# Optimization experiments

Hardware: AMD Instinct MI355X
Metric: run time of the kernel (lower is better)

The kernel has to match this reference:

```python
import jax, jax.numpy as jnp
import numpy as np

# dims: batch, seq, latent dims, embed dims, hidden, num_flows, vocab
B, S, D, E, H, F, V = 64, 2048, 64, 64, 512, 4, 32000


def setup_inputs() -> dict:
    key = jax.random.key(0)
    ks = jax.random.split(key, 10)
    z = jax.random.normal(ks[0], (B, S, D), jnp.float32)
    categ = jax.random.randint(ks[1], (B, S), 0, V)
    embed = jax.random.normal(ks[2], (V, E), jnp.float32) * 0.1
    # ExtActNorm nets: SimpleLinearLayer(embed_dims -> 2*num_dims), one per flow
    actnorm_W = jax.random.normal(ks[3], (F, E, 2 * D), jnp.float32) * (1.0 / np.sqrt(E))
    actnorm_b = jnp.zeros((F, 2 * D), jnp.float32)
    # Invertible 1x1 convs: near-identity init keeps exp/logdet well conditioned
    conv_W = jnp.eye(D, dtype=jnp.float32)[None] + 0.05 * jax.random.normal(ks[4], (F, D, D), jnp.float32)
    # Coupling layers: scaling_factor (zeros, per torch init) + LinearNet MLP
    scaling_factor = jnp.zeros((F, D), jnp.float32)
    W0 = jax.random.normal(ks[5], (F, D + E, H), jnp.float32) * (1.0 / np.sqrt(D + E))
    b0 = jnp.zeros((F, H), jnp.float32)
    W1 = jax.random.normal(ks[6], (F, H, H), jnp.float32) * (1.0 / np.sqrt(H))
    b1 = jnp.zeros((F, H), jnp.float32)
    W2 = jax.random.normal(ks[7], (F, H, 2 * D), jnp.float32) * (0.05 / np.sqrt(H))
    b2 = jnp.zeros((F, 2 * D), jnp.float32)
    return dict(z=z, categ=categ, embed=embed, actnorm_W=actnorm_W, actnorm_b=actnorm_b,
                conv_W=conv_W, scaling_factor=scaling_factor,
                W0=W0, b0=b0, W1=W1, b1=b1, W2=W2, b2=b2)


def reference(z, categ, embed, actnorm_W, actnorm_b, conv_W, scaling_factor,
              W0, b0, W1, b1, W2, b2):
    # channel mask: first floor(D/2) channels are the conditioning half
    c_masked = D // 2
    mask = jnp.concatenate([jnp.ones((c_masked,), z.dtype), jnp.zeros((D - c_masked,), z.dtype)])
    mask = mask[None, None, :]                     # [1,1,D]
    ext = embed[categ]                             # [B,S,E] category embeddings (ext_input)
    ldj = jnp.zeros((z.shape[0],), z.dtype)
    for f in range(F):
        # --- ExtActNormFlow: params predicted from embedding ---
        nn_out = jnp.einsum('bse,eo->bso', ext, actnorm_W[f]) + actnorm_b[f]
        bias, scales = jnp.split(nn_out, 2, axis=2)
        scales = jnp.tanh(scales)
        z = (z + bias) * jnp.exp(scales)
        ldj = ldj + scales.sum(axis=(1, 2))
        # --- InvertibleConv (1x1 over channels) ---
        z = jnp.einsum('bsd,de->bse', z, conv_W[f])
        _, logabsdet = jnp.linalg.slogdet(conv_W[f])
        ldj = ldj + z.shape[1] * logabsdet
        # --- CouplingLayer with LinearNet(z*mask, ext) ---
        z_in = z * mask
        h = jnp.concatenate([z_in, ext], axis=-1)            # [B,S,D+E]
        h = jax.nn.gelu(h @ W0[f] + b0[f], approximate=False)
        h = jax.nn.gelu(h @ W1[f] + b1[f], approximate=False)
        nn_out = h @ W2[f] + b2[f]                           # [B,S,2D]
        nn_out = nn_out.reshape(nn_out.shape[:-1] + (D, 2))
        s, t = nn_out[..., 0], nn_out[..., 1]
        sf = jnp.exp(scaling_factor[f]).reshape(1, 1, D)
        s = jnp.tanh(s / jnp.maximum(sf, 1.0)) * sf          # soft-clamped scale
        s = s * (1.0 - mask)
        t = t * (1.0 - mask)
        z = (z + t) * jnp.exp(s)
        ldj = ldj + s.sum(axis=(1, 2))
    return z, ldj
```

## Files before the change

### kernel.cpp

```cpp
#include <hip/hip_runtime.h>
#include <math.h>

#define BB 64
#define SS 2048
#define DD 64
#define EE 64
#define HH 512
#define FF 4
#define NTOK (BB*SS)
#define ZELEMS (NTOK*DD)

#define PK2 1376256
#define AN_PER_FLOW 24576

typedef float f32x4 __attribute__((ext_vector_type(4)));
typedef float f32x2 __attribute__((ext_vector_type(2)));
typedef short s16x8 __attribute__((ext_vector_type(8)));
typedef unsigned int u32x2 __attribute__((ext_vector_type(2)));

__device__ __forceinline__ short f2b(float x) {
  unsigned u = __float_as_uint(x);
  u += 0x7fffu + ((u >> 16) & 1u);
  return (short)(u >> 16);
}
__device__ __forceinline__ float b2f(short h) {
  return __uint_as_float(((unsigned)(unsigned short)h) << 16);
}
__device__ __forceinline__ unsigned cvt_pk_bf16(float a, float b) {
  unsigned r;
  asm("v_cvt_pk_bf16_f32 %0, %1, %2" : "=v"(r) : "v"(a), "v"(b));
  return r;
}

__device__ __forceinline__ float tanh_fast(float x) {
  float e = __expf(2.0f * x);
  return 1.0f - 2.0f * __builtin_amdgcn_rcpf(e + 1.0f);
}
__device__ __forceinline__ float gelu_fast(float x) {
  float u = x * x;
  float p = x * fmaf(0.07135481283f, u, 1.5957691216f);
  float e = __expf(-p);
  return x * __builtin_amdgcn_rcpf(1.0f + e);
}

__global__ __launch_bounds__(256) void pack_kernel(
    const float* __restrict__ W0, const float* __restrict__ W1,
    const float* __restrict__ W2, short* __restrict__ wp,
    float* __restrict__ ldj)
{
  int gid = blockIdx.x * 256 + threadIdx.x;
  if (gid < BB) ldj[gid] = 0.f;
  int f = gid / 43008;
  if (f >= FF) return;
  int rem = gid - f * 43008;
  int tile = rem >> 6, lane = rem & 63;
  int q = lane >> 4, c = lane & 15;
  short out[8];
  short* dst;
  if (tile < 96) {
    int kt = tile >> 5, nt = tile & 31;
    #pragma unroll
    for (int j = 0; j < 8; j++) {
      int k = kt*32 + q*8 + j;
      int row = (k < 32) ? k : k + 32;
      out[j] = f2b(W0[f*65536 + row*512 + nt*16 + c]);
    }
    dst = wp + f*344064 + (tile*64 + lane)*8;
  } else if (tile < 608) {
    int tl = tile - 96;
    int kt = tl >> 5, nt = tl & 31;
    #pragma unroll
    for (int j = 0; j < 8; j++) {
      int k = kt*32 + q*8 + j;
      out[j] = f2b(W1[f*262144 + k*512 + nt*16 + c]);
    }
    dst = wp + f*344064 + 49152 + (tl*64 + lane)*8;
  } else {
    int tl = tile - 608;
    int kt = tl >> 2, nt = tl & 3;
    #pragma unroll
    for (int j = 0; j < 8; j++) {
      int k = kt*32 + q*8 + j;
      out[j] = f2b(W2[f*65536 + k*128 + 64 + nt*16 + c]);
    }
    dst = wp + f*344064 + 311296 + (tl*64 + lane)*8;
  }
  *(s16x8*)dst = *(s16x8*)out;
}

__global__ __launch_bounds__(256) void pack2_kernel(
    const float* __restrict__ Wa, const float* __restrict__ Wc,
    short* __restrict__ wp)
{
  int gid = blockIdx.x * 256 + threadIdx.x;
  int f = gid / 1536;
  if (f >= FF) return;
  int rem = gid - f * 1536;
  int u = rem >> 6, lane = rem & 63;
  int q = lane >> 4, c = lane & 15;
  short hi[8], lo[8];
  short* base = wp + PK2 + f*AN_PER_FLOW;
  short* dh; short* dl;
  if (u < 16) {
    int kt = u >> 3, nt = u & 7;
    #pragma unroll
    for (int j = 0; j < 8; j++) {
      float v = Wa[f*8192 + (kt*32 + q*8 + j)*128 + nt*16 + c];
      hi[j] = f2b(v);
      lo[j] = f2b(v - b2f(hi[j]));
    }
    dh = base + u*512 + lane*8;
    dl = base + 8192 + u*512 + lane*8;
  } else {
    int uc = u - 16;
    int kt = uc >> 2, nt = uc & 3;
    #pragma unroll
    for (int j = 0; j < 8; j++) {
      float v = Wc[f*4096 + (kt*32 + q*8 + j)*64 + nt*16 + c];
      hi[j] = f2b(v);
      lo[j] = f2b(v - b2f(hi[j]));
    }
    dh = base + 16384 + uc*512 + lane*8;
    dl = base + 16384 + 4096 + uc*512 + lane*8;
  }
  *(s16x8*)dh = *(s16x8*)hi;
  *(s16x8*)dl = *(s16x8*)lo;
}

__global__ __launch_bounds__(64) void slogdet_kernel(
    const float* __restrict__ convW, float* __restrict__ ldj)
{
  __shared__ float A[64*65];
  const int f = blockIdx.x;
  const int t = threadIdx.x;
  for (int i = 0; i < 64; i++) A[i*65 + t] = convW[f*4096 + i*64 + t];
  __syncthreads();
  float lad = 0.f;
  for (int k = 0; k < 64; k++) {
    float v = (t >= k) ? fabsf(A[t*65 + k]) : -1.f;
    int p = t;
    #pragma unroll
    for (int off = 32; off; off >>= 1) {
      float ov = __shfl_down(v, off);
      int  op = __shfl_down(p, off);
      if (ov > v) { v = ov; p = op; }
    }
    p = __shfl(p, 0);
    __syncthreads();
    if (p != k) {
      float tmp = A[k*65 + t];
      A[k*65 + t] = A[p*65 + t];
      A[p*65 + t] = tmp;
    }
    __syncthreads();
    float piv = A[k*65 + k];
    lad += logf(fabsf(piv));
    float m = (t > k) ? A[t*65 + k] / piv : 0.f;
    __syncthreads();
    if (t > k) {
      for (int c = k+1; c < 64; c++)
        A[t*65 + c] = fmaf(-m, A[k*65 + c], A[t*65 + c]);
    }
    __syncthreads();
  }
  atomicAdd(&ldj[t], (float)SS * lad);
}

__global__ __launch_bounds__(512, 4) void flow_kernel(
    const float* __restrict__ z_in, float* __restrict__ zout,
    const int* __restrict__ categ, const float* __restrict__ embed,
    const float* __restrict__ ba, const short* __restrict__ wp,
    const float* __restrict__ b0, const float* __restrict__ b1,
    const float* __restrict__ b2, const float* __restrict__ scal,
    float* __restrict__ ldj)
{
  extern __shared__ char smem[];
  float* zf = (float*)smem;
  short* hs = (short*)(smem + 16384);
  short* ExtH = hs;
  short* ExtL = hs + 4096;
  short* ehp  = hs + 8192;
  short* elp  = hs + 12288;
  short* zb   = hs + 16384;

  const int t    = threadIdx.x;
  const int tok0 = blockIdx.x * 64;
  const int lane = t & 63;
  const int w    = __builtin_amdgcn_readfirstlane(t >> 6);
  const int q    = lane >> 4, c16 = lane & 15;
  const int swz  = (c16 & 7) << 3;
  const int zswz = (c16 & 7) << 2;
  const f32x4 vzero = {0.f, 0.f, 0.f, 0.f};

  #pragma unroll
  for (int it = 0; it < 2; it++) {
    int idx = t + it*512;
    int r = idx >> 4, c4 = (idx & 15) * 4;
    f32x4 v = *(const f32x4*)&z_in[(tok0 + r)*64 + c4];
    *(f32x4*)&zf[r*64 + (c4 ^ ((r & 7) << 2))] = v;
  }

  float lsum = 0.f;

  for (int f = 0; f < FF; f++) {
    const short* base = wp + PK2 + f*AN_PER_FLOW;
    const short* w0p  = wp + f*344064;
    const short* w1p  = w0p + 49152;
    const short* w2p  = w0p + 311296;

    __syncthreads();

    #pragma unroll
    for (int it = 0; it < 2; it++) {
      int idx = t + it*512;
      int r = idx >> 4, c4 = (idx & 15) * 4;
      int sw = (r & 7) << 3;
      f32x4 v = *(const f32x4*)&embed[categ[tok0 + r]*64 + c4];
      unsigned h01 = cvt_pk_bf16(v[0], v[1]);
      unsigned h23 = cvt_pk_bf16(v[2], v[3]);
      float r0 = v[0] - __uint_as_float(h01 << 16);
      float r1 = v[1] - __uint_as_float(h01 & 0xffff0000u);
      float r2 = v[2] - __uint_as_float(h23 << 16);
      float r3 = v[3] - __uint_as_float(h23 & 0xffff0000u);
      u32x2 hv = {h01, h23};
      u32x2 lv = {cvt_pk_bf16(r0, r1), cvt_pk_bf16(r2, r3)};
      *(u32x2*)&ExtH[r*64 + (c4 ^ sw)] = hv;
      *(u32x2*)&ExtL[r*64 + (c4 ^ sw)] = lv;
    }
    __syncthreads();

    const int ntb  = w & 3;
    const int rowg = w >> 2;
    const int db   = ntb*16 + q*4;

    f32x4 aB[2], aS[2];
    aB[0] = vzero; aB[1] = vzero; aS[0] = vzero; aS[1] = vzero;
    #pragma unroll
    for (int kt = 0; kt < 2; kt++) {
      s16x8 bhB = *(const s16x8*)&base[(kt*8 + ntb)*512 + lane*8];
      s16x8 blB = *(const s16x8*)&base[8192 + (kt*8 + ntb)*512 + lane*8];
      s16x8 bhS = *(const s16x8*)&base[(kt*8 + ntb + 4)*512 + lane*8];
      s16x8 blS = *(const s16x8*)&base[8192 + (kt*8 + ntb + 4)*512 + lane*8];
      #pragma unroll
      for (int r = 0; r < 2; r++) {
        int row = (rowg*2 + r)*16 + c16;
        s16x8 ah = *(const s16x8*)&ExtH[row*64 + ((kt*32 + q*8) ^ swz)];
        s16x8 al = *(const s16x8*)&ExtL[row*64 + ((kt*32 + q*8) ^ swz)];
        aB[r] = __builtin_amdgcn_mfma_f32_16x16x32_bf16(bhB, ah, aB[r], 0,0,0);
        aB[r] = __builtin_amdgcn_mfma_f32_16x16x32_bf16(blB, ah, aB[r], 0,0,0);
        aB[r] = __builtin_amdgcn_mfma_f32_16x16x32_bf16(bhB, al, aB[r], 0,0,0);
        aS[r] = __builtin_amdgcn_mfma_f32_16x16x32_bf16(bhS, ah, aS[r], 0,0,0);
        aS[r] = __builtin_amdgcn_mfma_f32_16x16x32_bf16(blS, ah, aS[r], 0,0,0);
        aS[r] = __builtin_amdgcn_mfma_f32_16x16x32_bf16(bhS, al, aS[r], 0,0,0);
      }
    }

    {
      f32x4 bB4 = *(const f32x4*)&ba[f*128 + db];
      f32x4 bS4 = *(const f32x4*)&ba[f*128 + 64 + db];
      #pragma unroll
      for (int r = 0; r < 2; r++) {
        int row = (rowg*2 + r)*16 + c16;
        f32x4 zv = *(const f32x4*)&zf[row*64 + (db ^ zswz)];
        float zp[4];
        #pragma unroll
        for (int i = 0; i < 4; i++) {
          float s = tanh_fast(aS[r][i] + bS4[i]);
          lsum += s;
          zp[i] = (zv[i] + aB[r][i] + bB4[i]) * __expf(s);
        }
        unsigned h01 = cvt_pk_bf16(zp[0], zp[1]);
        unsigned h23 = cvt_pk_bf16(zp[2], zp[3]);
        float r0 = zp[0] - __uint_as_float(h01 << 16);
        float r1 = zp[1] - __uint_as_float(h01 & 0xffff0000u);
        float r2 = zp[2] - __uint_as_float(h23 << 16);
        float r3 = zp[3] - __uint_as_float(h23 & 0xffff0000u);
        u32x2 hv = {h01, h23};
        u32x2 lv = {cvt_pk_bf16(r0, r1), cvt_pk_bf16(r2, r3)};
        *(u32x2*)&ehp[row*64 + (db ^ swz)] = hv;
        *(u32x2*)&elp[row*64 + (db ^ swz)] = lv;
      }
    }
    __syncthreads();

    {
      f32x4 ac[2];
      ac[0] = vzero; ac[1] = vzero;
      #pragma unroll
      for (int kt = 0; kt < 2; kt++) {
        s16x8 bh = *(const s16x8*)&base[16384 + (kt*4 + ntb)*512 + lane*8];
        s16x8 bl = *(const s16x8*)&base[16384 + 4096 + (kt*4 + ntb)*512 + lane*8];
        #pragma unroll
        for (int r = 0; r < 2; r++) {
          int row = (rowg*2 + r)*16 + c16;
          s16x8 ah = *(const s16x8*)&ehp[row*64 + ((kt*32 + q*8) ^ swz)];
          s16x8 al = *(const s16x8*)&elp[row*64 + ((kt*32 + q*8) ^ swz)];
          ac[r] = __builtin_amdgcn_mfma_f32_16x16x32_bf16(bh, ah, ac[r], 0,0,0);
          ac[r] = __builtin_amdgcn_mfma_f32_16x16x32_bf16(bl, ah, ac[r], 0,0,0);
          ac[r] = __builtin_amdgcn_mfma_f32_16x16x32_bf16(bh, al, ac[r], 0,0,0);
        }
      }
      #pragma unroll
      for (int r = 0; r < 2; r++) {
        int row = (rowg*2 + r)*16 + c16;
        *(f32x4*)&zf[row*64 + (db ^ zswz)] = ac[r];
        u32x2 pv = {cvt_pk_bf16(ac[r][0], ac[r][1]),
                    cvt_pk_bf16(ac[r][2], ac[r][3])};
        *(u32x2*)&zb[row*64 + (db ^ swz)] = pv;
      }
    }
    __syncthreads();

    f32x4 acc[4][4];

    #pragma unroll
    for (int rt = 0; rt < 4; rt++)
      #pragma unroll
      for (int nl = 0; nl < 4; nl++) acc[rt][nl] = vzero;
    #pragma unroll
    for (int kt = 0; kt < 3; kt++) {
      s16x8 a[4];
      #pragma unroll
      for (int rt = 0; rt < 4; rt++) {
        int row = rt*16 + c16;
        a[rt] = (kt == 0)
          ? *(const s16x8*)&zb[row*64 + ((q*8) ^ swz)]
          : *(const s16x8*)&ExtH[row*64 + (((kt-1)*32 + q*8) ^ swz)];
      }
      #pragma unroll
      for (int nl = 0; nl < 4; nl++) {
        s16x8 b = *(const s16x8*)&w0p[((kt*32 + w*4 + nl)*64 + lane)*8];
        #pragma unroll
        for (int rt = 0; rt < 4; rt++)
          acc[rt][nl] = __builtin_amdgcn_mfma_f32_16x16x32_bf16(b, a[rt], acc[rt][nl], 0,0,0);
      }
    }
    __syncthreads();
    #pragma unroll
    for (int nl = 0; nl < 4; nl++) {
      int nt = w*4 + nl;
      f32x4 bias = *(const f32x4*)&b0[f*512 + nt*16 + q*4];
      #pragma unroll
      for (int rt = 0; rt < 4; rt++) {
        float g0 = gelu_fast(acc[rt][nl][0] + bias[0]);
        float g1 = gelu_fast(acc[rt][nl][1] + bias[1]);
        float g2 = gelu_fast(acc[rt][nl][2] + bias[2]);
        float g3 = gelu_fast(acc[rt][nl][3] + bias[3]);
        u32x2 pv = {cvt_pk_bf16(g0, g1), cvt_pk_bf16(g2, g3)};
        *(u32x2*)&hs[(rt*16 + c16)*512 + ((nt*16 + q*4) ^ swz)] = pv;
      }
    }
    __syncthreads();

    #pragma unroll
    for (int rt = 0; rt < 4; rt++)
      #pragma unroll
      for (int nl = 0; nl < 4; nl++) acc[rt][nl] = vzero;
    {
      s16x8 bcur[4];
      #pragma unroll
      for (int nl = 0; nl < 4; nl++)
        bcur[nl] = *(const s16x8*)&w1p[((w*4 + nl)*64 + lane)*8];
      #pragma unroll 2
      for (int kt = 0; kt < 16; kt++) {
        const int ktn = (kt + 1) & 15;
        s16x8 a[4];
        #pragma unroll
        for (int rt = 0; rt < 4; rt++)
          a[rt] = *(const s16x8*)&hs[(rt*16 + c16)*512 + ((kt*32 + q*8) ^ swz)];
        #pragma unroll
        for (int nl = 0; nl < 4; nl++) {
          s16x8 bn = *(const s16x8*)&w1p[((ktn*32 + w*4 + nl)*64 + lane)*8];
          #pragma unroll
          for (int rt = 0; rt < 4; rt++)
            acc[rt][nl] = __builtin_amdgcn_mfma_f32_16x16x32_bf16(bcur[nl], a[rt], acc[rt][nl], 0,0,0);
          bcur[nl] = bn;
        }
      }
    }
    __syncthreads();
    #pragma unroll
    for (int nl = 0; nl < 4; nl++) {
      int nt = w*4 + nl;
      f32x4 bias = *(const f32x4*)&b1[f*512 + nt*16 + q*4];
      #pragma unroll
      for (int rt = 0; rt < 4; rt++) {
        float g0 = gelu_fast(acc[rt][nl][0] + bias[0]);
        float g1 = gelu_fast(acc[rt][nl][1] + bias[1]);
        float g2 = gelu_fast(acc[rt][nl][2] + bias[2]);
        float g3 = gelu_fast(acc[rt][nl][3] + bias[3]);
        u32x2 pv = {cvt_pk_bf16(g0, g1), cvt_pk_bf16(g2, g3)};
        *(u32x2*)&hs[(rt*16 + c16)*512 + ((nt*16 + q*4) ^ swz)] = pv;
      }
    }
    __syncthreads();

    {
      const int ntc = w & 3;
      const int rtb = w >> 2;
      f32x4 a2[2];
      a2[0] = vzero; a2[1] = vzero;
      s16x8 b2cur = *(const s16x8*)&w2p[(ntc*64 + lane)*8];
      #pragma unroll 2
      for (int kt = 0; kt < 16; kt++) {
        const int ktn = (kt + 1) & 15;
        s16x8 b2nxt = *(const s16x8*)&w2p[((ktn*4 + ntc)*64 + lane)*8];
        s16x8 x0 = *(const s16x8*)&hs[(rtb*16 + c16)*512 + ((kt*32 + q*8) ^ swz)];
        s16x8 x1 = *(const s16x8*)&hs[((rtb + 2)*16 + c16)*512 + ((kt*32 + q*8) ^ swz)];
        a2[0] = __builtin_amdgcn_mfma_f32_16x16x32_bf16(b2cur, x0, a2[0], 0,0,0);
        a2[1] = __builtin_amdgcn_mfma_f32_16x16x32_bf16(b2cur, x1, a2[1], 0,0,0);
        b2cur = b2nxt;
      }
      const int ccb = 64 + ntc*16 + q*4;
      f32x4 b2v = *(const f32x4*)&b2[f*128 + ccb];
      const int d0 = ccb >> 1;
      f32x2 sc = *(const f32x2*)&scal[f*64 + d0];
      float sf0 = __expf(sc[0]); float mr0 = __builtin_amdgcn_rcpf(fmaxf(sf0, 1.0f));
      float sf1 = __expf(sc[1]); float mr1 = __builtin_amdgcn_rcpf(fmaxf(sf1, 1.0f));
      #pragma unroll
      for (int u = 0; u < 2; u++) {
        int row = (rtb + u*2)*16 + c16;
        int zi = row*64 + (d0 ^ zswz);
        f32x2 zv = *(f32x2*)&zf[zi];
        float s0 = tanh_fast((a2[u][0] + b2v[0]) * mr0) * sf0;
        float s1 = tanh_fast((a2[u][2] + b2v[2]) * mr1) * sf1;
        zv[0] = (zv[0] + (a2[u][1] + b2v[1])) * __expf(s0);
        zv[1] = (zv[1] + (a2[u][3] + b2v[3])) * __expf(s1);
        *(f32x2*)&zf[zi] = zv;
        lsum += s0 + s1;
      }
    }
  }

  __syncthreads();

  #pragma unroll
  for (int it = 0; it < 2; it++) {
    int idx = t + it*512;
    int r = idx >> 4, c4 = (idx & 15) * 4;
    f32x4 v = *(const f32x4*)&zf[r*64 + (c4 ^ ((r & 7) << 2))];
    *(f32x4*)&zout[(tok0 + r)*64 + c4] = v;
  }

  #pragma unroll
  for (int off = 32; off; off >>= 1) lsum += __shfl_xor(lsum, off);
  if (lane == 0) atomicAdd(&ldj[tok0 >> 11], lsum);
}

extern "C" void kernel_launch(void* const* d_in, const int* in_sizes, int n_in,
                              void* d_out, int out_size, void* d_ws, size_t ws_size,
                              hipStream_t stream) {
  (void)in_sizes; (void)n_in; (void)out_size; (void)ws_size;
  const float* z_in  = (const float*)d_in[0];
  const int*   categ = (const int*)  d_in[1];
  const float* embed = (const float*)d_in[2];
  const float* Wa    = (const float*)d_in[3];
  const float* ba    = (const float*)d_in[4];
  const float* Wc    = (const float*)d_in[5];
  const float* scal  = (const float*)d_in[6];
  const float* W0    = (const float*)d_in[7];
  const float* b0    = (const float*)d_in[8];
  const float* W1    = (const float*)d_in[9];
  const float* b1    = (const float*)d_in[10];
  const float* W2    = (const float*)d_in[11];
  const float* b2    = (const float*)d_in[12];

  float* zbuf = (float*)d_out;
  float* ldj  = zbuf + ZELEMS;
  short* wp   = (short*)d_ws;

  hipFuncSetAttribute(reinterpret_cast<const void*>(flow_kernel),
                      hipFuncAttributeMaxDynamicSharedMemorySize, 81920);

  pack_kernel<<<672, 256, 0, stream>>>(W0, W1, W2, wp, ldj);
  pack2_kernel<<<24, 256, 0, stream>>>(Wa, Wc, wp);
  slogdet_kernel<<<4, 64, 0, stream>>>(Wc, ldj);
  flow_kernel<<<NTOK/64, 512, 81920, stream>>>(
      z_in, zbuf, categ, embed, ba, wp, b0, b1, b2, scal, ldj);
}
```

Baseline: 1.029 ms.

## Split MLP row tiles into two passes to halve accumulator registers

The layer-0 and layer-1 GEMMs now run in two passes of 32 rows each with 2x4 accumulators instead of one pass over 64 rows with 4x4, which cuts live accumulator registers to help the occupancy target of the launch bounds. The bf16 copy of z is dropped and converted on the fly from the fp32 z buffer, and the shared-memory regions for ext and z are moved. In exchange, weight fragments for layers 0 and 1 are loaded twice per flow, and the layer-1 pass must sync before writing into the shared hidden buffer that the other pass still reads.

```diff
diff --git a/kernel.cpp b/kernel.cpp
--- a/kernel.cpp
+++ b/kernel.cpp
@@ -177,11 +177,10 @@
   extern __shared__ char smem[];
   float* zf = (float*)smem;
   short* hs = (short*)(smem + 16384);
-  short* ExtH = hs;
-  short* ExtL = hs + 4096;
-  short* ehp  = hs + 8192;
-  short* elp  = hs + 12288;
-  short* zb   = hs + 16384;
+  short* ehp  = hs + 16384;
+  short* ExtH = hs + 20480;
+  short* ExtL = hs + 24576;
+  short* elp  = hs + 28672;
 
   const int t    = threadIdx.x;
   const int tok0 = blockIdx.x * 64;
@@ -304,59 +303,69 @@
       for (int r = 0; r < 2; r++) {
         int row = (rowg*2 + r)*16 + c16;
         *(f32x4*)&zf[row*64 + (db ^ zswz)] = ac[r];
-        u32x2 pv = {cvt_pk_bf16(ac[r][0], ac[r][1]),
-                    cvt_pk_bf16(ac[r][2], ac[r][3])};
-        *(u32x2*)&zb[row*64 + (db ^ swz)] = pv;
-      }
-    }
-    __syncthreads();
-
-    f32x4 acc[4][4];
-
-    #pragma unroll
-    for (int rt = 0; rt < 4; rt++)
-      #pragma unroll
-      for (int nl = 0; nl < 4; nl++) acc[rt][nl] = vzero;
-    #pragma unroll
-    for (int kt = 0; kt < 3; kt++) {
-      s16x8 a[4];
-      #pragma unroll
-      for (int rt = 0; rt < 4; rt++) {
-        int row = rt*16 + c16;
-        a[rt] = (kt == 0)
-          ? *(const s16x8*)&zb[row*64 + ((q*8) ^ swz)]
-          : *(const s16x8*)&ExtH[row*64 + (((kt-1)*32 + q*8) ^ swz)];
-      }
+      }
+    }
+    __syncthreads();
+
+    #pragma unroll 1
+    for (int pass = 0; pass < 2; pass++) {
+      f32x4 acc[2][4];
+      #pragma unroll
+      for (int rt = 0; rt < 2; rt++)
+        #pragma unroll
+        for (int nl = 0; nl < 4; nl++) acc[rt][nl] = vzero;
+      #pragma unroll
+      for (int kt = 0; kt < 3; kt++) {
+        s16x8 a[2];
+        #pragma unroll
+        for (int rt = 0; rt < 2; rt++) {
+          int row = (pass*2 + rt)*16 + c16;
+          if (kt == 0) {
+            f32x4 v0 = *(const f32x4*)&zf[row*64 + ((q*8) ^ zswz)];
+            f32x4 v1 = *(const f32x4*)&zf[row*64 + ((q*8 + 4) ^ zswz)];
+            union { unsigned u[4]; s16x8 v; } cv;
+            cv.u[0] = cvt_pk_bf16(v0[0], v0[1]);
+            cv.u[1] = cvt_pk_bf16(v0[2], v0[3]);
+            cv.u[2] = cvt_pk_bf16(v1[0], v1[1]);
+            cv.u[3] = cvt_pk_bf16(v1[2], v1[3]);
+            a[rt] = cv.v;
+          } else {
+            a[rt] = *(const s16x8*)&ExtH[row*64 + (((kt-1)*32 + q*8) ^ swz)];
+          }
+        }
+        #pragma unroll
+        for (int nl = 0; nl < 4; nl++) {
+          s16x8 b = *(const s16x8*)&w0p[((kt*32 + w*4 + nl)*64 + lane)*8];
+          acc[0][nl] = __builtin_amdgcn_mfma_f32_16x16x32_bf16(b, a[0], acc[0][nl], 0,0,0);
+          acc[1][nl] = __builtin_amdgcn_mfma_f32_16x16x32_bf16(b, a[1], acc[1][nl], 0,0,0);
+        }
+      }
+      if (pass == 1) __syncthreads();
       #pragma unroll
       for (int nl = 0; nl < 4; nl++) {
-        s16x8 b = *(const s16x8*)&w0p[((kt*32 + w*4 + nl)*64 + lane)*8];
-        #pragma unroll
-        for (int rt = 0; rt < 4; rt++)
-          acc[rt][nl] = __builtin_amdgcn_mfma_f32_16x16x32_bf16(b, a[rt], acc[rt][nl], 0,0,0);
-      }
-    }
-    __syncthreads();
-    #pragma unroll
-    for (int nl = 0; nl < 4; nl++) {
-      int nt = w*4 + nl;
-      f32x4 bias = *(const f32x4*)&b0[f*512 + nt*16 + q*4];
-      #pragma unroll
-      for (int rt = 0; rt < 4; rt++) {
-        float g0 = gelu_fast(acc[rt][nl][0] + bias[0]);
-        float g1 = gelu_fast(acc[rt][nl][1] + bias[1]);
-        float g2 = gelu_fast(acc[rt][nl][2] + bias[2]);
-        float g3 = gelu_fast(acc[rt][nl][3] + bias[3]);
-        u32x2 pv = {cvt_pk_bf16(g0, g1), cvt_pk_bf16(g2, g3)};
-        *(u32x2*)&hs[(rt*16 + c16)*512 + ((nt*16 + q*4) ^ swz)] = pv;
-      }
-    }
-    __syncthreads();
-
-    #pragma unroll
-    for (int rt = 0; rt < 4; rt++)
-      #pragma unroll
-      for (int nl = 0; nl < 4; nl++) acc[rt][nl] = vzero;
-    {
+        int nt = w*4 + nl;
+        f32x4 bias = *(const f32x4*)&b0[f*512 + nt*16 + q*4];
+        #pragma unroll
+        for (int rt = 0; rt < 2; rt++) {
+          int row = (pass*2 + rt)*16 + c16;
+          float g0 = gelu_fast(acc[rt][nl][0] + bias[0]);
+          float g1 = gelu_fast(acc[rt][nl][1] + bias[1]);
+          float g2 = gelu_fast(acc[rt][nl][2] + bias[2]);
+          float g3 = gelu_fast(acc[rt][nl][3] + bias[3]);
+          u32x2 pv = {cvt_pk_bf16(g0, g1), cvt_pk_bf16(g2, g3)};
+          *(u32x2*)&hs[row*512 + ((nt*16 + q*4) ^ swz)] = pv;
+        }
+      }
+    }
+    __syncthreads();
+
+    #pragma unroll 1
+    for (int pass = 0; pass < 2; pass++) {
+      f32x4 acc[2][4];
+      #pragma unroll
+      for (int rt = 0; rt < 2; rt++)
+        #pragma unroll
+        for (int nl = 0; nl < 4; nl++) acc[rt][nl] = vzero;
       s16x8 bcur[4];
       #pragma unroll
       for (int nl = 0; nl < 4; nl++)
@@ -364,33 +373,33 @@
       #pragma unroll 2
       for (int kt = 0; kt < 16; kt++) {
         const int ktn = (kt + 1) & 15;
-        s16x8 a[4];
-        #pragma unroll
-        for (int rt = 0; rt < 4; rt++)
-          a[rt] = *(const s16x8*)&hs[(rt*16 + c16)*512 + ((kt*32 + q*8) ^ swz)];
+        s16x8 a[2];
+        #pragma unroll
+        for (int rt = 0; rt < 2; rt++)
+          a[rt] = *(const s16x8*)&hs[((pass*2 + rt)*16 + c16)*512 + ((kt*32 + q*8) ^ swz)];
         #pragma unroll
         for (int nl = 0; nl < 4; nl++) {
           s16x8 bn = *(const s16x8*)&w1p[((ktn*32 + w*4 + nl)*64 + lane)*8];
-          #pragma unroll
-          for (int rt = 0; rt < 4; rt++)
-            acc[rt][nl] = __builtin_amdgcn_mfma_f32_16x16x32_bf16(bcur[nl], a[rt], acc[rt][nl], 0,0,0);
+          acc[0][nl] = __builtin_amdgcn_mfma_f32_16x16x32_bf16(bcur[nl], a[0], acc[0][nl], 0,0,0);
+          acc[1][nl] = __builtin_amdgcn_mfma_f32_16x16x32_bf16(bcur[nl], a[1], acc[1][nl], 0,0,0);
           bcur[nl] = bn;
         }
       }
-    }
-    __syncthreads();
-    #pragma unroll
-    for (int nl = 0; nl < 4; nl++) {
-      int nt = w*4 + nl;
-      f32x4 bias = *(const f32x4*)&b1[f*512 + nt*16 + q*4];
-      #pragma unroll
-      for (int rt = 0; rt < 4; rt++) {
-        float g0 = gelu_fast(acc[rt][nl][0] + bias[0]);
-        float g1 = gelu_fast(acc[rt][nl][1] + bias[1]);
-        float g2 = gelu_fast(acc[rt][nl][2] + bias[2]);
-        float g3 = gelu_fast(acc[rt][nl][3] + bias[3]);
-        u32x2 pv = {cvt_pk_bf16(g0, g1), cvt_pk_bf16(g2, g3)};
-        *(u32x2*)&hs[(rt*16 + c16)*512 + ((nt*16 + q*4) ^ swz)] = pv;
+      __syncthreads();
+      #pragma unroll
+      for (int nl = 0; nl < 4; nl++) {
+        int nt = w*4 + nl;
+        f32x4 bias = *(const f32x4*)&b1[f*512 + nt*16 + q*4];
+        #pragma unroll
+        for (int rt = 0; rt < 2; rt++) {
+          int row = (pass*2 + rt)*16 + c16;
+          float g0 = gelu_fast(acc[rt][nl][0] + bias[0]);
+          float g1 = gelu_fast(acc[rt][nl][1] + bias[1]);
+          float g2 = gelu_fast(acc[rt][nl][2] + bias[2]);
+          float g3 = gelu_fast(acc[rt][nl][3] + bias[3]);
+          u32x2 pv = {cvt_pk_bf16(g0, g1), cvt_pk_bf16(g2, g3)};
+          *(u32x2*)&hs[row*512 + ((nt*16 + q*4) ^ swz)] = pv;
+        }
       }
     }
     __syncthreads();
```

Result: slower. 1.130 ms (+9.8%).
